# Kernel tuning notes

Measured on AMD Instinct MI355X. Metric: run time of the kernel, lower is better.

Reference implementation:

```python
import jax, jax.numpy as jnp
import numpy as np

K = 5                 # neighbours kept (select_knn uses K+1 incl. self, col 0 dropped)
SCORE_THRESHOLD = 0.5
BIG = 1.0e9           # sentinel used by the original for invalid (-1) neighbours


def setup_inputs() -> dict:
    key = jax.random.key(0)
    k1, k2 = jax.random.split(key)
    B, S, D = 16, 4096, 3          # 16 events of 4096 hits
    N = B * S
    coords = jax.random.normal(k1, (N, D), dtype=jnp.float32)
    score = jax.random.uniform(k2, (N, 1), dtype=jnp.float32)
    rs = jnp.arange(B + 1, dtype=jnp.int32) * S   # uniform row splits
    return {"score": score, "coords": coords, "rs": rs}


def _graph_condensation(score, coords, rs):
    N, D = coords.shape
    B = rs.shape[0] - 1
    S = N // B                      # uniform row splits by construction

    # direction: 0 = can only BE neighbour (high score), 1 = can only HAVE neighbours
    direction = jnp.where(score[:, 0] > SCORE_THRESHOLD, 0, 1)   # [N]

    # safeguard: threshold = min(0.98 * min over events of per-event max score, thr)
    mrss = jnp.max(score[:, 0].reshape(B, S), axis=1)            # [B]
    thr_eff = jnp.minimum(jnp.min(mrss) * jnp.float32(0.98),
                          jnp.float32(SCORE_THRESHOLD))

    # selected (promoted) vertices; static-shape representation of ragged mask:
    sel_mask = score[:, 0] >= thr_eff                            # [N] bool
    counts = jnp.sum(sel_mask.reshape(B, S), axis=1)
    rs_up = jnp.concatenate([jnp.zeros(1, jnp.int32),
                             jnp.cumsum(counts).astype(jnp.int32)])  # [B+1]

    # --- directional KNN within each event (dense faithful version of select_knn) ---
    x = coords.reshape(B, S, D)
    xx = jnp.sum(x * x, axis=-1)                                 # [B,S]
    d2 = xx[:, :, None] + xx[:, None, :] - 2.0 * jnp.einsum('bsd,btd->bst', x, x)
    d2 = jnp.maximum(d2, 0.0)                                    # [B,S,S]

    cand = (direction == 0).reshape(B, S)                        # may-be-neighbour
    eye = jnp.eye(S, dtype=bool)                                 # exclude self (col 0 dropped in orig)
    d2m = jnp.where(cand[:, None, :] & ~eye[None], d2, BIG)

    negv, idx = jax.lax.top_k(-d2m, K)                           # K nearest candidates
    dist = -negv                                                 # [B,S,K] squared dists
    nidx = idx.astype(jnp.int32) + (jnp.arange(B, dtype=jnp.int32) * S)[:, None, None]

    query = (direction == 1).reshape(B, S)                       # may-have-neighbours
    valid = query[:, :, None] & (dist < BIG)
    nidx = jnp.where(valid, nidx, -1).reshape(N, K)
    dist = jnp.where(valid, dist, 0.0).reshape(N, K)             # dist=0 where nidx<0

    # argsort-based reorder exactly as in the original (invalid pushed to the end)
    ssc = jnp.where(nidx < 0, BIG, dist)
    order = jnp.argsort(ssc, axis=1)
    nidx = jnp.take_along_axis(nidx, order, axis=1)
    dist = jnp.take_along_axis(dist, order, axis=1)

    dist = jax.lax.stop_gradient(dist)
    weights = jax.nn.softmax(jnp.exp(-dist), axis=-1)            # [N,K]

    return nidx, dist, weights, rs_up, sel_mask


def reference(score, coords, rs):
    nidx_down, distsq_down, weights_down, rs_up, sel_mask = _graph_condensation(score, coords, rs)
    return (nidx_down, distsq_down, weights_down, rs_up, sel_mask)
```

## Files before the change

kernel.cpp:

```cpp
#include <hip/hip_runtime.h>
#include <math.h>

#define S      4096
#define BEV    16
#define KNN    5
#define BIGF   1.0e9f
#define NSL    32
#define GPP    8
#define NTH    256
#define RSTR   81

__device__ __forceinline__ float fmulrn(float a, float b) { return __fmul_rn(a, b); }
__device__ __forceinline__ float faddrn(float a, float b) { return __fadd_rn(a, b); }

__global__ __launch_bounds__(1024) void k_scan(const float* __restrict__ score,
                                               float* __restrict__ mrss4,
                                               int* __restrict__ qn, int* __restrict__ cn) {
    int blk = blockIdx.x, t = threadIdx.x;
    int b = blk >> 2, ch = blk & 3;
    float v = score[(size_t)b * S + ch * 1024 + t];
    float m = v;
    int pk = (v > 0.5f) ? (1 << 16) : 1;
#pragma unroll
    for (int off = 32; off >= 1; off >>= 1) {
        m = fmaxf(m, __shfl_xor(m, off, 64));
        pk += __shfl_xor(pk, off, 64);
    }
    __shared__ float wm[16];
    __shared__ int wp[16];
    int wid = t >> 6;
    if ((t & 63) == 0) { wm[wid] = m; wp[wid] = pk; }
    __syncthreads();
    if (t == 0) {
        float mm = wm[0]; int pp = wp[0];
        for (int w = 1; w < 16; w++) { mm = fmaxf(mm, wm[w]); pp += wp[w]; }
        mrss4[blk] = mm;
        qn[blk] = pp & 0xffff;
        cn[blk] = pp >> 16;
    }
}

__global__ void k_off(const float* __restrict__ mrss4,
                      const int* __restrict__ qn, const int* __restrict__ cn,
                      float* __restrict__ thrv,
                      int* __restrict__ qchoff, int* __restrict__ cchoff,
                      int* __restrict__ qcount, int* __restrict__ ccount,
                      int* __restrict__ qpoff) {
    if (threadIdx.x != 0) return;
    float mn = 3.0e38f;
    for (int b = 0; b < BEV; b++) {
        float mx = mrss4[b * 4];
        for (int ch = 1; ch < 4; ch++) mx = fmaxf(mx, mrss4[b * 4 + ch]);
        mn = fminf(mn, mx);
    }
    thrv[0] = fminf(__fmul_rn(mn, 0.98f), 0.5f);
    int qp = 0;
    for (int b = 0; b < BEV; b++) {
        int qq = 0, cc = 0;
        for (int ch = 0; ch < 4; ch++) {
            qchoff[b * 4 + ch] = qq; cchoff[b * 4 + ch] = cc;
            qq += qn[b * 4 + ch];    cc += cn[b * 4 + ch];
        }
        qcount[b] = qq; ccount[b] = cc;
        qpoff[b] = qp; qp += (qq + 1) >> 1;
    }
    qpoff[BEV] = qp;
}

__global__ __launch_bounds__(1024) void k_sel(const float* __restrict__ score,
                                              const float* __restrict__ coords,
                                              const float* __restrict__ thrv,
                                              const int* __restrict__ qchoff,
                                              const int* __restrict__ cchoff,
                                              int* __restrict__ scount,
                                              int* __restrict__ qlist,
                                              int* __restrict__ clist,
                                              float4* __restrict__ qpts,
                                              float4* __restrict__ ptsc,
                                              float* __restrict__ out_nidx,
                                              float* __restrict__ out_dist,
                                              float* __restrict__ out_w,
                                              float* __restrict__ out_sel) {
    int blk = blockIdx.x, t = threadIdx.x;
    int b = blk >> 2, ch = blk & 3;
    int p = ch * 1024 + t;
    size_t gi = (size_t)b * S + p;
    float v = score[gi];
    float thr = thrv[0];
    out_sel[gi] = (v >= thr) ? 1.0f : 0.0f;
    bool cand = (v > 0.5f);
    int pk = cand ? (1 << 16) : 1;
    int incl = pk;
#pragma unroll
    for (int off = 1; off < 64; off <<= 1) {
        int u = __shfl_up(incl, off, 64);
        if ((t & 63) >= off) incl += u;
    }
    __shared__ int wtot[16];
    __shared__ int wsel[16];
    int wid = t >> 6;
    if ((t & 63) == 63) wtot[wid] = incl;
    int sel = (v >= thr) ? 1 : 0;
#pragma unroll
    for (int off = 32; off >= 1; off >>= 1) sel += __shfl_xor(sel, off, 64);
    if ((t & 63) == 0) wsel[wid] = sel;
    __syncthreads();
    int base = 0;
    for (int w = 0; w < wid; w++) base += wtot[w];
    int excl = base + incl - pk;
    if (t == 0) {
        int sc2 = 0;
        for (int w = 0; w < 16; w++) sc2 += wsel[w];
        scount[blk] = sc2;
    }
    const float* c = coords + gi * 3;
    float x = c[0], y = c[1], z = c[2];
    float xx = faddrn(faddrn(fmulrn(x, x), fmulrn(y, y)), fmulrn(z, z));
    size_t ebase = (size_t)b * S;
    if (cand) {
        int pos = cchoff[blk] + (excl >> 16);
        clist[ebase + pos] = p;
        ptsc[ebase + pos] = make_float4(fmulrn(-2.0f, x), fmulrn(-2.0f, y),
                                        fmulrn(-2.0f, z), xx);
#pragma unroll
        for (int k = 0; k < KNN; k++) {
            out_nidx[gi * KNN + k] = -1.0f;
            out_dist[gi * KNN + k] = 0.0f;
            out_w[gi * KNN + k]    = 0.2f;
        }
    } else {
        int pos = qchoff[blk] + (excl & 0xffff);
        qlist[ebase + pos] = p;
        qpts[ebase + pos] = make_float4(x, y, z, xx);
    }
}

__global__ __launch_bounds__(NTH, 4) void k_knn(const float4* __restrict__ ptsc,
                                                const float4* __restrict__ qpts,
                                                const int* __restrict__ qlist,
                                                const int* __restrict__ clist,
                                                const int* __restrict__ qpoff,
                                                const int* __restrict__ qcount,
                                                const int* __restrict__ ccount,
                                                const int* __restrict__ scount,
                                                float* __restrict__ out_nidx,
                                                float* __restrict__ out_dist,
                                                float* __restrict__ out_w,
                                                float* __restrict__ out_rsup) {
    int pg = blockIdx.x, t = threadIdx.x;
    if (pg == 0 && t == 0) {
        int acc = 0;
        out_rsup[0] = 0.0f;
        for (int e = 0; e < BEV; e++) {
            acc += scount[e * 4] + scount[e * 4 + 1] + scount[e * 4 + 2] + scount[e * 4 + 3];
            out_rsup[e + 1] = (float)acc;
        }
    }
    int total = qpoff[BEV];
    if (pg * GPP >= total) return;

    __shared__ int sqp[BEV + 1];
    __shared__ int sqc[BEV];
    __shared__ int scc[BEV];
    __shared__ float dpart[NSL * RSTR];
    __shared__ unsigned short ipart[NSL * RSTR];
    if (t < BEV + 1) sqp[t] = qpoff[t];
    if (t < BEV) { sqc[t] = qcount[t]; scc[t] = ccount[t]; }
    __syncthreads();

    int pr = t & (GPP - 1), sl = t >> 3;
    int gpr = pg * GPP + pr;
    bool pact = gpr < total;
    int gp = pact ? gpr : (total - 1);
    int b = 0;
#pragma unroll
    for (int e = 1; e < BEV; e++) b += (gp >= sqp[e]) ? 1 : 0;
    int rp = gp - sqp[b];
    int qc = sqc[b], cc = scc[b];
    int r0 = 2 * rp, r1 = r0 + 1;
    bool a1v = pact && (r1 < qc);
    size_t ebase = (size_t)b * S;
    float4 q0 = qpts[ebase + r0];
    float4 q1 = qpts[ebase + (a1v ? r1 : r0)];

    int slen = (cc + NSL - 1) / NSL;
    int j0 = sl * slen;
    int j1 = min(j0 + slen, cc);

    const float INF = __int_as_float(0x7f800000);
    float A0=INF,A1=INF,A2=INF,A3=INF,A4=INF; int IA0=-1,IA1=-1,IA2=-1,IA3=-1,IA4=-1;
    float B0=INF,B1=INF,B2=INF,B3=INF,B4=INF; int IB0=-1,IB1=-1,IB2=-1,IB3=-1,IB4=-1;
    const float4* __restrict__ pp = ptsc + ebase;

#pragma unroll 4
    for (int j = j0; j < j1; j++) {
        float4 p = pp[j];
        float dm0 = faddrn(faddrn(fmulrn(p.x, q0.x), fmulrn(p.y, q0.y)), fmulrn(p.z, q0.z));
        float dd0 = fmaxf(faddrn(faddrn(q0.w, p.w), dm0), 0.0f);
        float dm1 = faddrn(faddrn(fmulrn(p.x, q1.x), fmulrn(p.y, q1.y)), fmulrn(p.z, q1.z));
        float dd1 = fmaxf(faddrn(faddrn(q1.w, p.w), dm1), 0.0f);
        {
            bool c0=dd0<A0,c1=dd0<A1,c2=dd0<A2,c3=dd0<A3,c4=dd0<A4;
            IA4=c4?(c3?IA3:j):IA4; IA3=c3?(c2?IA2:j):IA3; IA2=c2?(c1?IA1:j):IA2;
            IA1=c1?(c0?IA0:j):IA1; IA0=c0?j:IA0;
            A4=__builtin_amdgcn_fmed3f(dd0,A3,A4); A3=__builtin_amdgcn_fmed3f(dd0,A2,A3);
            A2=__builtin_amdgcn_fmed3f(dd0,A1,A2); A1=__builtin_amdgcn_fmed3f(dd0,A0,A1);
            A0=fminf(A0,dd0);
        }
        {
            bool c0=dd1<B0,c1=dd1<B1,c2=dd1<B2,c3=dd1<B3,c4=dd1<B4;
            IB4=c4?(c3?IB3:j):IB4; IB3=c3?(c2?IB2:j):IB3; IB2=c2?(c1?IB1:j):IB2;
            IB1=c1?(c0?IB0:j):IB1; IB0=c0?j:IB0;
            B4=__builtin_amdgcn_fmed3f(dd1,B3,B4); B3=__builtin_amdgcn_fmed3f(dd1,B2,B3);
            B2=__builtin_amdgcn_fmed3f(dd1,B1,B2); B1=__builtin_amdgcn_fmed3f(dd1,B0,B1);
            B0=fminf(B0,dd1);
        }
    }

    float* wd = &dpart[sl * RSTR + pr * 10];
    unsigned short* wi = &ipart[sl * RSTR + pr * 10];
    wd[0]=A0; wd[1]=A1; wd[2]=A2; wd[3]=A3; wd[4]=A4;
    wd[5]=B0; wd[6]=B1; wd[7]=B2; wd[8]=B3; wd[9]=B4;
    wi[0]=(unsigned short)(IA0-j0); wi[1]=(unsigned short)(IA1-j0);
    wi[2]=(unsigned short)(IA2-j0); wi[3]=(unsigned short)(IA3-j0);
    wi[4]=(unsigned short)(IA4-j0);
    wi[5]=(unsigned short)(IB0-j0); wi[6]=(unsigned short)(IB1-j0);
    wi[7]=(unsigned short)(IB2-j0); wi[8]=(unsigned short)(IB3-j0);
    wi[9]=(unsigned short)(IB4-j0);
    __syncthreads();

    if (t < 2 * GPP) {
        int pr2 = t >> 1, rs = t & 1;
        int gpr2 = pg * GPP + pr2;
        bool pact2 = gpr2 < total;
        int gp2 = pact2 ? gpr2 : (total - 1);
        int b2 = 0;
#pragma unroll
        for (int e = 1; e < BEV; e++) b2 += (gp2 >= sqp[e]) ? 1 : 0;
        int rp2 = gp2 - sqp[b2];
        int qc2 = sqc[b2], cc2 = scc[b2];
        int slen2 = (cc2 + NSL - 1) / NSL;
        int r = 2 * rp2 + rs;
        bool valid = pact2 && (r < qc2);

        unsigned long long a0=~0ull, a1u=~0ull, a2u=~0ull, a3u=~0ull, a4u=~0ull;
        for (int s2 = 0; s2 < NSL; s2++) {
            const float* dp = &dpart[s2 * RSTR + pr2 * 10 + rs * 5];
            const unsigned short* ip = &ipart[s2 * RSTR + pr2 * 10 + rs * 5];
#pragma unroll
            for (int k = 0; k < KNN; k++) {
                float d = dp[k];
                unsigned int jj = (unsigned int)(s2 * slen2 + (int)ip[k]);
                unsigned long long key = ((unsigned long long)__float_as_uint(d) << 32) | jj;
                if (key < a4u) {
                    a4u = key;
                    if (a4u < a3u) { unsigned long long u = a3u; a3u = a4u; a4u = u; }
                    if (a3u < a2u) { unsigned long long u = a2u; a2u = a3u; a3u = u; }
                    if (a2u < a1u) { unsigned long long u = a1u; a1u = a2u; a2u = u; }
                    if (a1u < a0)  { unsigned long long u = a0;  a0  = a1u; a1u = u; }
                }
            }
        }
        if (valid) {
            size_t eb2 = (size_t)b2 * S;
            int irow = qlist[eb2 + r];
            size_t gi = eb2 + irow;
            unsigned long long av[KNN] = {a0, a1u, a2u, a3u, a4u};
            float dk[KNN], nk[KNN], ev[KNN];
            float m = -3.0e38f;
#pragma unroll
            for (int k = 0; k < KNN; k++) {
                float d = __uint_as_float((unsigned int)(av[k] >> 32));
                bool val = (d < BIGF);
                int cpos = (int)(unsigned int)(av[k] & 0xffffffffu);
                if (!val || cpos >= S || cpos < 0) cpos = 0;
                dk[k] = val ? d : 0.0f;
                nk[k] = val ? (float)(b2 * S + clist[eb2 + cpos]) : -1.0f;
                ev[k] = expf(-dk[k]);
                m = fmaxf(m, ev[k]);
            }
            float u[KNN], ssum = 0.0f;
#pragma unroll
            for (int k = 0; k < KNN; k++) { u[k] = expf(ev[k] - m); ssum += u[k]; }
#pragma unroll
            for (int k = 0; k < KNN; k++) {
                out_nidx[gi * KNN + k] = nk[k];
                out_dist[gi * KNN + k] = dk[k];
                out_w[gi * KNN + k]    = u[k] / ssum;
            }
        }
    }
}

extern "C" void kernel_launch(void* const* d_in, const int* in_sizes, int n_in,
                              void* d_out, int out_size, void* d_ws, size_t ws_size,
                              hipStream_t stream) {
    const float* score  = (const float*)d_in[0];
    const float* coords = (const float*)d_in[1];

    float* out = (float*)d_out;
    size_t NK = (size_t)BEV * S * KNN;
    float* out_nidx = out;
    float* out_dist = out + NK;
    float* out_w    = out + 2 * NK;
    float* out_rsup = out + 3 * NK;
    float* out_sel  = out + 3 * NK + (BEV + 1);

    char* ws = (char*)d_ws;
    float* mrss4  = (float*)(ws + 0);
    int* qn       = (int*)(ws + 256);
    int* cn       = (int*)(ws + 512);
    int* qchoff   = (int*)(ws + 768);
    int* cchoff   = (int*)(ws + 1024);
    int* qcount   = (int*)(ws + 1280);
    int* ccount   = (int*)(ws + 1344);
    int* qpoff    = (int*)(ws + 1408);
    int* scount   = (int*)(ws + 1536);
    float* thrv   = (float*)(ws + 1792);
    int* qlist    = (int*)(ws + 2048);
    int* clist    = (int*)(ws + 2048 + (size_t)BEV * S * 4);
    float4* qpts  = (float4*)(ws + 2048 + (size_t)BEV * S * 8);
    float4* ptsc  = (float4*)(ws + 2048 + (size_t)BEV * S * 8 + (size_t)BEV * S * 16);

    k_scan<<<BEV * 4, 1024, 0, stream>>>(score, mrss4, qn, cn);
    k_off<<<1, 64, 0, stream>>>(mrss4, qn, cn, thrv, qchoff, cchoff,
                                qcount, ccount, qpoff);
    k_sel<<<BEV * 4, 1024, 0, stream>>>(score, coords, thrv, qchoff, cchoff, scount,
                                        qlist, clist, qpts, ptsc,
                                        out_nidx, out_dist, out_w, out_sel);
    k_knn<<<(BEV * ((S + 1) / 2) + GPP - 1) / GPP, NTH, 0, stream>>>(
        ptsc, qpts, qlist, clist, qpoff, qcount, ccount, scount,
        out_nidx, out_dist, out_w, out_rsup);
}
```

Before: 97.25 us.

## Stage per-event candidate points in LDS and align query pairs to block boundaries

Pads each event's query-pair range to a multiple of GPP so every KNN block belongs to a single event, simplifying event lookup. Each block then cooperatively copies the event's candidate points into shared memory in a slice-interleaved layout, and the distance loop reads from LDS instead of global memory, with a global fallback beyond EMAX. This trades extra LDS use (about 37 KB more per block, lowering occupancy) and a per-block staging pass for lower-latency candidate reads.

```diff
diff --git a/kernel.cpp b/kernel.cpp
--- a/kernel.cpp
+++ b/kernel.cpp
@@ -9,6 +9,7 @@
 #define GPP    8
 #define NTH    256
 #define RSTR   81
+#define EMAX   72
 
 __device__ __forceinline__ float fmulrn(float a, float b) { return __fmul_rn(a, b); }
 __device__ __forceinline__ float faddrn(float a, float b) { return __fadd_rn(a, b); }
@@ -62,7 +63,9 @@
             qq += qn[b * 4 + ch];    cc += cn[b * 4 + ch];
         }
         qcount[b] = qq; ccount[b] = cc;
-        qpoff[b] = qp; qp += (qq + 1) >> 1;
+        qpoff[b] = qp;
+        int pairs = (qq + 1) >> 1;
+        qp += ((pairs + GPP - 1) / GPP) * GPP;
     }
     qpoff[BEV] = qp;
 }
@@ -135,18 +138,33 @@
     }
 }
 
-__global__ __launch_bounds__(NTH, 4) void k_knn(const float4* __restrict__ ptsc,
-                                                const float4* __restrict__ qpts,
-                                                const int* __restrict__ qlist,
-                                                const int* __restrict__ clist,
-                                                const int* __restrict__ qpoff,
-                                                const int* __restrict__ qcount,
-                                                const int* __restrict__ ccount,
-                                                const int* __restrict__ scount,
-                                                float* __restrict__ out_nidx,
-                                                float* __restrict__ out_dist,
-                                                float* __restrict__ out_w,
-                                                float* __restrict__ out_rsup) {
+#define INSERT_A(dd, j) { \
+    bool c0=dd<A0,c1=dd<A1,c2=dd<A2,c3=dd<A3,c4=dd<A4; \
+    IA4=c4?(c3?IA3:j):IA4; IA3=c3?(c2?IA2:j):IA3; IA2=c2?(c1?IA1:j):IA2; \
+    IA1=c1?(c0?IA0:j):IA1; IA0=c0?j:IA0; \
+    A4=__builtin_amdgcn_fmed3f(dd,A3,A4); A3=__builtin_amdgcn_fmed3f(dd,A2,A3); \
+    A2=__builtin_amdgcn_fmed3f(dd,A1,A2); A1=__builtin_amdgcn_fmed3f(dd,A0,A1); \
+    A0=fminf(A0,dd); }
+#define INSERT_B(dd, j) { \
+    bool c0=dd<B0,c1=dd<B1,c2=dd<B2,c3=dd<B3,c4=dd<B4; \
+    IB4=c4?(c3?IB3:j):IB4; IB3=c3?(c2?IB2:j):IB3; IB2=c2?(c1?IB1:j):IB2; \
+    IB1=c1?(c0?IB0:j):IB1; IB0=c0?j:IB0; \
+    B4=__builtin_amdgcn_fmed3f(dd,B3,B4); B3=__builtin_amdgcn_fmed3f(dd,B2,B3); \
+    B2=__builtin_amdgcn_fmed3f(dd,B1,B2); B1=__builtin_amdgcn_fmed3f(dd,B0,B1); \
+    B0=fminf(B0,dd); }
+
+__global__ __launch_bounds__(NTH) void k_knn(const float4* __restrict__ ptsc,
+                                             const float4* __restrict__ qpts,
+                                             const int* __restrict__ qlist,
+                                             const int* __restrict__ clist,
+                                             const int* __restrict__ qpoff,
+                                             const int* __restrict__ qcount,
+                                             const int* __restrict__ ccount,
+                                             const int* __restrict__ scount,
+                                             float* __restrict__ out_nidx,
+                                             float* __restrict__ out_dist,
+                                             float* __restrict__ out_w,
+                                             float* __restrict__ out_rsup) {
     int pg = blockIdx.x, t = threadIdx.x;
     if (pg == 0 && t == 0) {
         int acc = 0;
@@ -160,61 +178,65 @@
     if (pg * GPP >= total) return;
 
     __shared__ int sqp[BEV + 1];
-    __shared__ int sqc[BEV];
-    __shared__ int scc[BEV];
+    __shared__ int sqcv[2 * BEV];
+    __shared__ float4 spts[EMAX * NSL];
     __shared__ float dpart[NSL * RSTR];
     __shared__ unsigned short ipart[NSL * RSTR];
     if (t < BEV + 1) sqp[t] = qpoff[t];
-    if (t < BEV) { sqc[t] = qcount[t]; scc[t] = ccount[t]; }
+    if (t < BEV) { sqcv[t] = qcount[t]; sqcv[BEV + t] = ccount[t]; }
+    __syncthreads();
+
+    int gp0 = pg * GPP;
+    int b = 0;
+#pragma unroll
+    for (int e = 1; e < BEV; e++) b += (gp0 >= sqp[e]) ? 1 : 0;
+    int qc = sqcv[b], cc = sqcv[BEV + b];
+    size_t ebase = (size_t)b * S;
+    const float4* __restrict__ pp = ptsc + ebase;
+    int slen = (cc + NSL - 1) / NSL;
+
+    for (int jj2 = t; jj2 < cc; jj2 += NTH) {
+        int slj = (int)((unsigned)jj2 / (unsigned)slen);
+        int ej = jj2 - slj * slen;
+        if (ej < EMAX) spts[ej * NSL + slj] = pp[jj2];
+    }
     __syncthreads();
 
     int pr = t & (GPP - 1), sl = t >> 3;
-    int gpr = pg * GPP + pr;
-    bool pact = gpr < total;
-    int gp = pact ? gpr : (total - 1);
-    int b = 0;
-#pragma unroll
-    for (int e = 1; e < BEV; e++) b += (gp >= sqp[e]) ? 1 : 0;
-    int rp = gp - sqp[b];
-    int qc = sqc[b], cc = scc[b];
+    int rp = gp0 + pr - sqp[b];
     int r0 = 2 * rp, r1 = r0 + 1;
-    bool a1v = pact && (r1 < qc);
-    size_t ebase = (size_t)b * S;
-    float4 q0 = qpts[ebase + r0];
-    float4 q1 = qpts[ebase + (a1v ? r1 : r0)];
-
-    int slen = (cc + NSL - 1) / NSL;
+    bool p0v = (unsigned)r0 < (unsigned)qc;
+    bool p1v = (unsigned)r1 < (unsigned)qc;
+    float4 q0 = qpts[ebase + (p0v ? r0 : 0)];
+    float4 q1 = qpts[ebase + (p1v ? r1 : (p0v ? r0 : 0))];
+
     int j0 = sl * slen;
     int j1 = min(j0 + slen, cc);
+    int n1 = min(j1 - j0, EMAX); if (n1 < 0) n1 = 0;
 
     const float INF = __int_as_float(0x7f800000);
     float A0=INF,A1=INF,A2=INF,A3=INF,A4=INF; int IA0=-1,IA1=-1,IA2=-1,IA3=-1,IA4=-1;
     float B0=INF,B1=INF,B2=INF,B3=INF,B4=INF; int IB0=-1,IB1=-1,IB2=-1,IB3=-1,IB4=-1;
-    const float4* __restrict__ pp = ptsc + ebase;
-
+
+    int j = j0;
 #pragma unroll 4
-    for (int j = j0; j < j1; j++) {
+    for (int e = 0; e < n1; ++e, ++j) {
+        float4 p = spts[e * NSL + sl];
+        float dm0 = faddrn(faddrn(fmulrn(p.x, q0.x), fmulrn(p.y, q0.y)), fmulrn(p.z, q0.z));
+        float dd0 = fmaxf(faddrn(faddrn(q0.w, p.w), dm0), 0.0f);
+        float dm1 = faddrn(faddrn(fmulrn(p.x, q1.x), fmulrn(p.y, q1.y)), fmulrn(p.z, q1.z));
+        float dd1 = fmaxf(faddrn(faddrn(q1.w, p.w), dm1), 0.0f);
+        INSERT_A(dd0, j)
+        INSERT_B(dd1, j)
+    }
+    for (; j < j1; ++j) {
         float4 p = pp[j];
         float dm0 = faddrn(faddrn(fmulrn(p.x, q0.x), fmulrn(p.y, q0.y)), fmulrn(p.z, q0.z));
         float dd0 = fmaxf(faddrn(faddrn(q0.w, p.w), dm0), 0.0f);
         float dm1 = faddrn(faddrn(fmulrn(p.x, q1.x), fmulrn(p.y, q1.y)), fmulrn(p.z, q1.z));
         float dd1 = fmaxf(faddrn(faddrn(q1.w, p.w), dm1), 0.0f);
-        {
-            bool c0=dd0<A0,c1=dd0<A1,c2=dd0<A2,c3=dd0<A3,c4=dd0<A4;
-            IA4=c4?(c3?IA3:j):IA4; IA3=c3?(c2?IA2:j):IA3; IA2=c2?(c1?IA1:j):IA2;
-            IA1=c1?(c0?IA0:j):IA1; IA0=c0?j:IA0;
-            A4=__builtin_amdgcn_fmed3f(dd0,A3,A4); A3=__builtin_amdgcn_fmed3f(dd0,A2,A3);
-            A2=__builtin_amdgcn_fmed3f(dd0,A1,A2); A1=__builtin_amdgcn_fmed3f(dd0,A0,A1);
-            A0=fminf(A0,dd0);
-        }
-        {
-            bool c0=dd1<B0,c1=dd1<B1,c2=dd1<B2,c3=dd1<B3,c4=dd1<B4;
-            IB4=c4?(c3?IB3:j):IB4; IB3=c3?(c2?IB2:j):IB3; IB2=c2?(c1?IB1:j):IB2;
-            IB1=c1?(c0?IB0:j):IB1; IB0=c0?j:IB0;
-            B4=__builtin_amdgcn_fmed3f(dd1,B3,B4); B3=__builtin_amdgcn_fmed3f(dd1,B2,B3);
-            B2=__builtin_amdgcn_fmed3f(dd1,B1,B2); B1=__builtin_amdgcn_fmed3f(dd1,B0,B1);
-            B0=fminf(B0,dd1);
-        }
+        INSERT_A(dd0, j)
+        INSERT_B(dd1, j)
     }
 
     float* wd = &dpart[sl * RSTR + pr * 10];
@@ -231,17 +253,9 @@
 
     if (t < 2 * GPP) {
         int pr2 = t >> 1, rs = t & 1;
-        int gpr2 = pg * GPP + pr2;
-        bool pact2 = gpr2 < total;
-        int gp2 = pact2 ? gpr2 : (total - 1);
-        int b2 = 0;
-#pragma unroll
-        for (int e = 1; e < BEV; e++) b2 += (gp2 >= sqp[e]) ? 1 : 0;
-        int rp2 = gp2 - sqp[b2];
-        int qc2 = sqc[b2], cc2 = scc[b2];
-        int slen2 = (cc2 + NSL - 1) / NSL;
+        int rp2 = gp0 + pr2 - sqp[b];
         int r = 2 * rp2 + rs;
-        bool valid = pact2 && (r < qc2);
+        bool valid = (unsigned)r < (unsigned)qc;
 
         unsigned long long a0=~0ull, a1u=~0ull, a2u=~0ull, a3u=~0ull, a4u=~0ull;
         for (int s2 = 0; s2 < NSL; s2++) {
@@ -250,7 +264,7 @@
 #pragma unroll
             for (int k = 0; k < KNN; k++) {
                 float d = dp[k];
-                unsigned int jj = (unsigned int)(s2 * slen2 + (int)ip[k]);
+                unsigned int jj = (unsigned int)(s2 * slen + (int)ip[k]);
                 unsigned long long key = ((unsigned long long)__float_as_uint(d) << 32) | jj;
                 if (key < a4u) {
                     a4u = key;
@@ -262,9 +276,8 @@
             }
         }
         if (valid) {
-            size_t eb2 = (size_t)b2 * S;
-            int irow = qlist[eb2 + r];
-            size_t gi = eb2 + irow;
+            int irow = qlist[ebase + r];
+            size_t gi = ebase + irow;
             unsigned long long av[KNN] = {a0, a1u, a2u, a3u, a4u};
             float dk[KNN], nk[KNN], ev[KNN];
             float m = -3.0e38f;
@@ -275,7 +288,7 @@
                 int cpos = (int)(unsigned int)(av[k] & 0xffffffffu);
                 if (!val || cpos >= S || cpos < 0) cpos = 0;
                 dk[k] = val ? d : 0.0f;
-                nk[k] = val ? (float)(b2 * S + clist[eb2 + cpos]) : -1.0f;
+                nk[k] = val ? (float)(b * S + clist[ebase + cpos]) : -1.0f;
                 ev[k] = expf(-dk[k]);
                 m = fmaxf(m, ev[k]);
             }
@@ -328,7 +341,7 @@
     k_sel<<<BEV * 4, 1024, 0, stream>>>(score, coords, thrv, qchoff, cchoff, scount,
                                         qlist, clist, qpts, ptsc,
                                         out_nidx, out_dist, out_w, out_sel);
-    k_knn<<<(BEV * ((S + 1) / 2) + GPP - 1) / GPP, NTH, 0, stream>>>(
+    k_knn<<<(BEV * (S / 2) + GPP - 1) / GPP, NTH, 0, stream>>>(
         ptsc, qpts, qlist, clist, qpoff, qcount, ccount, scount,
         out_nidx, out_dist, out_w, out_rsup);
 }
```

Result: slower. 118.9 us (+22.2%).
